# Kernel tuning notes

Hardware: AMD Instinct MI355X
Metric: run time of the kernel (lower is better)

Reference implementation:

```python
import jax, jax.numpy as jnp
import numpy as np

D_MODEL = 1024
NUM_HEADS = 16
D_K = D_MODEL // NUM_HEADS

def setup_inputs() -> dict:
    key = jax.random.key(0)
    ks = jax.random.split(key, 8)
    B, S, D = 2, 2048, D_MODEL
    scale = 1.0 / np.sqrt(D)
    return {
        "X_q": jax.random.normal(ks[0], (B, S, D), dtype=jnp.float32),
        "X_k": jax.random.normal(ks[1], (B, S, D), dtype=jnp.float32),
        "X_v": jax.random.normal(ks[2], (B, S, D), dtype=jnp.float32),
        "W_q": jax.random.normal(ks[3], (D, D), dtype=jnp.float32) * scale,
        "W_k": jax.random.normal(ks[4], (D, D), dtype=jnp.float32) * scale,
        "W_v": jax.random.normal(ks[5], (D, D), dtype=jnp.float32) * scale,
        "W_o": jax.random.normal(ks[6], (D, D), dtype=jnp.float32) * scale,
        "b_o": jnp.zeros((D,), dtype=jnp.float32),
    }

def reference(X_q, X_k, X_v, W_q, W_k, W_v, W_o, b_o):
    B, S, D = X_q.shape
    H, dk = NUM_HEADS, D_K
    # nn.Linear: x @ W.T
    Q = (X_q @ W_q.T).reshape(B, H, S, dk)  # faithful raw view, no transpose
    K = (X_k @ W_k.T).reshape(B, H, S, dk)
    V = (X_v @ W_v.T).reshape(B, H, S, dk)
    A = jnp.einsum("bhqd,bhkd->bhqk", Q, K) / np.sqrt(dk)  # [B,H,S,S]
    A = jax.nn.softmax(A, axis=-1)
    H_cat = jnp.einsum("bhqk,bhkd->bhqd", A, V).reshape(B, S, D)
    return H_cat @ W_o.T + b_o
```

## Files before the change

### kernel.cpp

```cpp
#include <hip/hip_runtime.h>

typedef __bf16 bf16;
typedef bf16 bf16x8 __attribute__((ext_vector_type(8)));
typedef bf16 bf16x4 __attribute__((ext_vector_type(4)));
typedef bf16 bf16x2 __attribute__((ext_vector_type(2)));
typedef float f32x4 __attribute__((ext_vector_type(4)));
typedef float f32x16 __attribute__((ext_vector_type(16)));
typedef int i32x4 __attribute__((ext_vector_type(4)));

#define XSZ 4194304
#define WSZ 1048576
#define KDIM 1024
#define QSCALE 0.1803368801111137f

__device__ __forceinline__ void async16(const bf16* g, bf16* l) {
  __builtin_amdgcn_global_load_lds(
      (const __attribute__((address_space(1))) unsigned int*)g,
      (__attribute__((address_space(3))) unsigned int*)l, 16, 0, 0);
}

__device__ __forceinline__ bf16x8 ld8(const bf16* p) {
  bf16x4 lo = *(const bf16x4*)p;
  bf16x4 hi = *(const bf16x4*)(p + 4);
  return __builtin_shufflevector(lo, hi, 0, 1, 2, 3, 4, 5, 6, 7);
}

__device__ __forceinline__ void st8s(bf16* p, bf16x8 v) {
  *(bf16x4*)p       = __builtin_shufflevector(v, v, 0, 1, 2, 3);
  *(bf16x4*)(p + 4) = __builtin_shufflevector(v, v, 4, 5, 6, 7);
}

__device__ __forceinline__ f32x4 mfma16(bf16x8 a, bf16x8 b, f32x4 c) {
  return __builtin_amdgcn_mfma_f32_16x16x32_bf16(a, b, c, 0, 0, 0);
}
__device__ __forceinline__ f32x16 mfma32(bf16x8 a, bf16x8 b, f32x16 c) {
  return __builtin_amdgcn_mfma_f32_32x32x16_bf16(a, b, c, 0, 0, 0);
}

__device__ __forceinline__ int packbf2(float lo, float hi) {
  bf16x2 t; t[0] = (bf16)lo; t[1] = (bf16)hi;
  return __builtin_bit_cast(int, t);
}

__device__ __forceinline__ float fast_exp2(float x) {
#if __has_builtin(__builtin_amdgcn_exp2f)
  return __builtin_amdgcn_exp2f(x);
#else
  return exp2f(x);
#endif
}


__global__ __launch_bounds__(256) void cast_all(const float* __restrict__ Xq, const float* __restrict__ Xk,
                                                const float* __restrict__ Xv, const float* __restrict__ Wq,
                                                const float* __restrict__ Wk, const float* __restrict__ Wv,
                                                const float* __restrict__ Wo, bf16* __restrict__ dst) {
  size_t i = ((size_t)blockIdx.x * 256 + threadIdx.x) * 8;
  const float* src; size_t off; float scale = 1.0f;
  if (i < XSZ)                { src = Xq; off = i; }
  else if (i < 2 * (size_t)XSZ) { src = Xk; off = i - XSZ; }
  else if (i < 3 * (size_t)XSZ) { src = Xv; off = i - 2 * (size_t)XSZ; }
  else if (i < 3 * (size_t)XSZ + WSZ) { src = Wq; off = i - 3 * (size_t)XSZ; scale = QSCALE; }
  else if (i < 3 * (size_t)XSZ + 2 * (size_t)WSZ) { src = Wk; off = i - 3 * (size_t)XSZ - WSZ; }
  else if (i < 3 * (size_t)XSZ + 3 * (size_t)WSZ) { src = Wv; off = i - 3 * (size_t)XSZ - 2 * (size_t)WSZ; }
  else                        { src = Wo; off = i - 3 * (size_t)XSZ - 3 * (size_t)WSZ; }
  float4 a = *(const float4*)(src + off);
  float4 b = *(const float4*)(src + off + 4);
  bf16x8 o;
  o[0] = (bf16)(a.x * scale); o[1] = (bf16)(a.y * scale);
  o[2] = (bf16)(a.z * scale); o[3] = (bf16)(a.w * scale);
  o[4] = (bf16)(b.x * scale); o[5] = (bf16)(b.y * scale);
  o[6] = (bf16)(b.z * scale); o[7] = (bf16)(b.w * scale);
  *(bf16x8*)(dst + i) = o;
}

__device__ __forceinline__ void gemm_nt_core(const bf16* __restrict__ A, const bf16* __restrict__ Bm,
                                             int m0, int n0, bf16* lds, f32x4 acc[4][4]) {
  const int t = threadIdx.x;
  const int lane = t & 63, wave = t >> 6;
  const int wm = wave & 1, wn = wave >> 1;
  const int quad = lane >> 4, m16 = lane & 15;
  bf16* As = lds;
  bf16* Bs = lds + 128 * 32;
  const int c0 = t, c1 = t + 256;
  const bf16* ga0 = A + (size_t)(m0 + (c0 >> 2)) * KDIM + (c0 & 3) * 8;
  const bf16* ga1 = A + (size_t)(m0 + (c1 >> 2)) * KDIM + (c1 & 3) * 8;
  const bf16* gb0 = Bm + (size_t)(n0 + (c0 >> 2)) * KDIM + (c0 & 3) * 8;
  const bf16* gb1 = Bm + (size_t)(n0 + (c1 >> 2)) * KDIM + (c1 & 3) * 8;
  for (int kt = 0; kt < KDIM; kt += 32) {
    async16(ga0 + kt, As + c0 * 8);
    async16(ga1 + kt, As + c1 * 8);
    async16(gb0 + kt, Bs + c0 * 8);
    async16(gb1 + kt, Bs + c1 * 8);
    __syncthreads();
    bf16x8 af[4], bfv[4];
    #pragma unroll
    for (int i = 0; i < 4; i++)
      af[i] = *(const bf16x8*)(As + (wm * 64 + i * 16 + m16) * 32 + quad * 8);
    #pragma unroll
    for (int i = 0; i < 4; i++)
      bfv[i] = *(const bf16x8*)(Bs + (wn * 64 + i * 16 + m16) * 32 + quad * 8);
    #pragma unroll
    for (int mi = 0; mi < 4; mi++)
      #pragma unroll
      for (int ni = 0; ni < 4; ni++)
        acc[mi][ni] = mfma16(af[mi], bfv[ni], acc[mi][ni]);
    __syncthreads();
  }
}

__global__ __launch_bounds__(256) void proj_gemm(const bf16* __restrict__ xq, const bf16* __restrict__ xk,
                                                 const bf16* __restrict__ xv, const bf16* __restrict__ wq,
                                                 const bf16* __restrict__ wk, const bf16* __restrict__ wv,
                                                 bf16* __restrict__ Qo, bf16* __restrict__ Ko,
                                                 bf16* __restrict__ Vo) {
  __shared__ bf16 lds[2 * 128 * 32];
  const int z = blockIdx.z;
  const bf16* A = (z == 0) ? xq : (z == 1) ? xk : xv;
  const bf16* W = (z == 0) ? wq : (z == 1) ? wk : wv;
  bf16* C = (z == 0) ? Qo : (z == 1) ? Ko : Vo;
  f32x4 acc[4][4];
  #pragma unroll
  for (int i = 0; i < 4; i++)
    #pragma unroll
    for (int j = 0; j < 4; j++) acc[i][j] = (f32x4){0.f, 0.f, 0.f, 0.f};
  gemm_nt_core(A, W, blockIdx.y * 128, blockIdx.x * 128, lds, acc);
  const int lane = threadIdx.x & 63, wave = threadIdx.x >> 6;
  const int wm = wave & 1, wn = wave >> 1, quad = lane >> 4, m16 = lane & 15;
  const int row0 = blockIdx.y * 128 + wm * 64;
  const int col0 = blockIdx.x * 128 + wn * 64;
  #pragma unroll
  for (int mi = 0; mi < 4; mi++)
    #pragma unroll
    for (int ni = 0; ni < 4; ni++)
      #pragma unroll
      for (int r = 0; r < 4; r++) {
        int row = row0 + mi * 16 + quad * 4 + r;
        int col = col0 + ni * 16 + m16;
        C[(size_t)row * 1024 + col] = (bf16)acc[mi][ni][r];
      }
}

__global__ __launch_bounds__(256) void out_gemm(const bf16* __restrict__ Hm, const bf16* __restrict__ wo,
                                                const float* __restrict__ bias, float* __restrict__ out) {
  __shared__ bf16 lds[128 * 32 + 64 * 32];
  bf16* As = lds;
  bf16* Bs = lds + 128 * 32;
  const int t = threadIdx.x;
  const int lane = t & 63, wave = t >> 6;
  const int wm = wave & 1, wn = wave >> 1;
  const int quad = lane >> 4, m16 = lane & 15;
  const int m0 = blockIdx.y * 128, n0 = blockIdx.x * 64;
  const int c0 = t, c1 = t + 256;
  const bf16* ga0 = Hm + (size_t)(m0 + (c0 >> 2)) * KDIM + (c0 & 3) * 8;
  const bf16* ga1 = Hm + (size_t)(m0 + (c1 >> 2)) * KDIM + (c1 & 3) * 8;
  const bf16* gb0 = wo + (size_t)(n0 + (c0 >> 2)) * KDIM + (c0 & 3) * 8;
  f32x4 acc[4][2];
  #pragma unroll
  for (int i = 0; i < 4; i++)
    #pragma unroll
    for (int j = 0; j < 2; j++) acc[i][j] = (f32x4){0.f, 0.f, 0.f, 0.f};
  for (int kt = 0; kt < KDIM; kt += 32) {
    async16(ga0 + kt, As + c0 * 8);
    async16(ga1 + kt, As + c1 * 8);
    if (c0 < 256) async16(gb0 + kt, Bs + c0 * 8);
    __syncthreads();
    bf16x8 af[4], bfv[2];
    #pragma unroll
    for (int i = 0; i < 4; i++)
      af[i] = *(const bf16x8*)(As + (wm * 64 + i * 16 + m16) * 32 + quad * 8);
    #pragma unroll
    for (int i = 0; i < 2; i++)
      bfv[i] = *(const bf16x8*)(Bs + (wn * 32 + i * 16 + m16) * 32 + quad * 8);
    #pragma unroll
    for (int mi = 0; mi < 4; mi++)
      #pragma unroll
      for (int ni = 0; ni < 2; ni++)
        acc[mi][ni] = mfma16(af[mi], bfv[ni], acc[mi][ni]);
    __syncthreads();
  }
  const int row0 = m0 + wm * 64;
  const int col0 = n0 + wn * 32;
  float bv[2];
  #pragma unroll
  for (int ni = 0; ni < 2; ni++) bv[ni] = bias[col0 + ni * 16 + m16];
  #pragma unroll
  for (int mi = 0; mi < 4; mi++)
    #pragma unroll
    for (int ni = 0; ni < 2; ni++)
      #pragma unroll
      for (int r = 0; r < 4; r++) {
        int row = row0 + mi * 16 + quad * 4 + r;
        int col = col0 + ni * 16 + m16;
        out[(size_t)row * 1024 + col] = acc[mi][ni][r] + bv[ni];
      }
}

__global__ __launch_bounds__(256) void transpose_v(const bf16* __restrict__ V, bf16* __restrict__ Vt) {
  __shared__ bf16 T[64 * 65];
  const int t = threadIdx.x;
  const bf16* src = V + (size_t)blockIdx.y * (2048 * 64) + (size_t)blockIdx.x * 64 * 64;
  bf16* dst = Vt + (size_t)blockIdx.y * (2048 * 64) + (size_t)blockIdx.x * 64;
  #pragma unroll
  for (int j = 0; j < 2; j++) {
    int c = t + j * 256;
    int row = c >> 3, col8 = (c & 7) * 8;
    bf16x8 v = *(const bf16x8*)(src + row * 64 + col8);
    #pragma unroll
    for (int i = 0; i < 8; i++) T[row * 65 + col8 + i] = v[i];
  }
  __syncthreads();
  #pragma unroll
  for (int j = 0; j < 2; j++) {
    int c = t + j * 256;
    int d = c >> 3, k8 = (c & 7) * 8;
    bf16x8 o;
    #pragma unroll
    for (int i = 0; i < 8; i++) o[i] = T[(k8 + i) * 65 + d];
    *(bf16x8*)(dst + (size_t)d * 2048 + k8) = o;
  }
}

#define KS 68
#define VS 132
#define HALF_LDS (128 * KS + 64 * VS)
__global__ __launch_bounds__(512, 2) void attn_kernel(const bf16* __restrict__ Qg,
                                                      const bf16* __restrict__ Kg,
                                                      const bf16* __restrict__ Vtg,
                                                      bf16* __restrict__ Hout) {
  __shared__ bf16 smem[2 * HALF_LDS];
  const int t = threadIdx.x;
  const int lane = t & 63;
  const int w = (t >> 6) & 3;
  const int half = t >> 8;
  const int tt = t & 255;
  const int l31 = lane & 31, h = lane >> 5;
  bf16* Ks = smem + half * HALF_LDS;
  bf16* Vs = Ks + 128 * KS;
  const int L = blockIdx.x + 16 * blockIdx.y;
  const int xcd = L & 7, j5 = L >> 3;
  const int bh = xcd * 4 + (j5 & 3);
  const int qt = j5 >> 2;
  const size_t base = (size_t)bh * (2048 * 64);
  const bf16* Kp = Kg + base;
  const bf16* Vp = Vtg + base;
  const int q = qt * 128 + w * 32 + l31;

  bf16x8 qf[4];
  #pragma unroll
  for (int kc = 0; kc < 4; kc++)
    qf[kc] = *(const bf16x8*)(Qg + base + (size_t)q * 64 + 16 * kc + 8 * h);

  f32x16 oacc[2];
  #pragma unroll
  for (int mt = 0; mt < 2; mt++)
    #pragma unroll
    for (int i = 0; i < 16; i++) oacc[mt][i] = 0.f;
  float lrow = 0.f;

  int krow[4], kcol[4], vrow[4], vcol[4];
  #pragma unroll
  for (int j = 0; j < 4; j++) {
    int c = tt + j * 256;
    krow[j] = c >> 3;  kcol[j] = (c & 7) * 8;
    vrow[j] = c >> 4;  vcol[j] = (c & 15) * 8;
  }

  const int tile0 = half * 8;
  bf16x8 kreg[4], vreg[4];
  #pragma unroll
  for (int j = 0; j < 4; j++) {
    kreg[j] = *(const bf16x8*)(Kp + (size_t)(tile0 * 128 + krow[j]) * 64 + kcol[j]);
    vreg[j] = *(const bf16x8*)(Vp + (size_t)vrow[j] * 2048 + tile0 * 128 + vcol[j]);
  }

  for (int kt = 0; kt < 8; kt++) {
    #pragma unroll
    for (int j = 0; j < 4; j++) st8s(Ks + krow[j] * KS + kcol[j], kreg[j]);
    #pragma unroll
    for (int j = 0; j < 4; j++) st8s(Vs + vrow[j] * VS + vcol[j], vreg[j]);
    __syncthreads();

    if (kt + 1 < 8) {
      const int tg = tile0 + kt + 1;
      #pragma unroll
      for (int j = 0; j < 4; j++) {
        kreg[j] = *(const bf16x8*)(Kp + (size_t)(tg * 128 + krow[j]) * 64 + kcol[j]);
        vreg[j] = *(const bf16x8*)(Vp + (size_t)vrow[j] * 2048 + tg * 128 + vcol[j]);
      }
    }

    #pragma unroll
    for (int mt = 0; mt < 4; mt++) {
      f32x16 sacc;
      #pragma unroll
      for (int i = 0; i < 16; i++) sacc[i] = 0.f;
      #pragma unroll
      for (int kc = 0; kc < 4; kc++) {
        bf16x8 kf = ld8(Ks + (32 * mt + l31) * KS + 16 * kc + 8 * h);
        sacc = mfma32(kf, qf[kc], sacc);
      }
      int pd[8];
      float sum = 0.f;
      #pragma unroll
      for (int p = 0; p < 8; p++) {
        float p0 = fast_exp2(sacc[2 * p]);
        float p1 = fast_exp2(sacc[2 * p + 1]);
        sum += p0 + p1;
        pd[p] = packbf2(p0, p1);
      }
      lrow += sum;
      #pragma unroll
      for (int c1 = 0; c1 < 2; c1++) {
        const int kc = 2 * mt + c1;
        const int rro = 2 * c1 + h;
        const int rrp = 2 * c1 + 1 - h;
        int s0 = __shfl_xor(pd[2 * rrp], 32, 64);
        int s1 = __shfl_xor(pd[2 * rrp + 1], 32, 64);
        int o0 = pd[2 * rro], o1 = pd[2 * rro + 1];
        i32x4 w4;
        w4.x = h ? s0 : o0;
        w4.y = h ? s1 : o1;
        w4.z = h ? o0 : s0;
        w4.w = h ? o1 : s1;
        bf16x8 pfrag = __builtin_bit_cast(bf16x8, w4);
        #pragma unroll
        for (int mtd = 0; mtd < 2; mtd++) {
          bf16x8 vf = ld8(Vs + (32 * mtd + l31) * VS + 16 * kc + 8 * h);
          oacc[mtd] = mfma32(vf, pfrag, oacc[mtd]);
        }
      }
    }
    __syncthreads();
  }

  lrow += __shfl_xor(lrow, 32, 64);
  float* Sf = (float*)smem;
  float* Tf = Sf + w * 2048;
  float* Lb = Sf + 8192 + w * 32;
  if (half) {
    #pragma unroll
    for (int mt = 0; mt < 2; mt++)
      #pragma unroll
      for (int r = 0; r < 16; r++) {
        int d = 32 * mt + (r & 3) + 8 * (r >> 2) + 4 * h;
        Tf[d * 32 + l31] = oacc[mt][r];
      }
    if (!h) Lb[l31] = lrow;
  }
  __syncthreads();
  if (!half) {
    float linv = 1.f / (lrow + Lb[l31]);
    #pragma unroll
    for (int mt = 0; mt < 2; mt++)
      #pragma unroll
      for (int r = 0; r < 16; r++) {
        int d = 32 * mt + (r & 3) + 8 * (r >> 2) + 4 * h;
        Tf[d * 32 + l31] = (oacc[mt][r] + Tf[d * 32 + l31]) * linv;
      }
  }
  __syncthreads();
  bf16* Hq = Hout + base + (size_t)(qt * 128 + w * 32 + l31) * 64 + 32 * h;
  #pragma unroll
  for (int s = 0; s < 2; s++) {
    int se = half * 2 + s;
    bf16x8 o;
    #pragma unroll
    for (int i = 0; i < 8; i++) o[i] = (bf16)Tf[(32 * h + se * 8 + i) * 32 + l31];
    *(bf16x8*)(Hq + se * 8) = o;
  }
}

extern "C" void kernel_launch(void* const* d_in, const int* in_sizes, int n_in,
                              void* d_out, int out_size, void* d_ws, size_t ws_size,
                              hipStream_t stream) {
  const float* Xq = (const float*)d_in[0];
  const float* Xk = (const float*)d_in[1];
  const float* Xv = (const float*)d_in[2];
  const float* Wq = (const float*)d_in[3];
  const float* Wk = (const float*)d_in[4];
  const float* Wv = (const float*)d_in[5];
  const float* Wo = (const float*)d_in[6];
  const float* bo = (const float*)d_in[7];

  bf16* ws = (bf16*)d_ws;
  bf16* xq = ws;
  bf16* xk = ws + XSZ;
  bf16* xv = ws + 2 * (size_t)XSZ;
  bf16* wq = ws + 3 * (size_t)XSZ;
  bf16* wk = wq + WSZ;
  bf16* wv = wk + WSZ;
  bf16* wo = wv + WSZ;
  bf16* q  = wo + WSZ;
  bf16* k  = q + XSZ;
  bf16* v  = k + XSZ;
  bf16* vt = xv;
  bf16* h  = xq;

  cast_all<<<8192, 256, 0, stream>>>(Xq, Xk, Xv, Wq, Wk, Wv, Wo, ws);
  proj_gemm<<<dim3(8, 32, 3), 256, 0, stream>>>(xq, xk, xv, wq, wk, wv, q, k, v);
  transpose_v<<<dim3(32, 32), 256, 0, stream>>>(v, vt);
  attn_kernel<<<dim3(16, 32), 512, 0, stream>>>(q, k, vt, h);
  out_gemm<<<dim3(16, 32), 256, 0, stream>>>(h, wo, bo, (float*)d_out);
}
```

Baseline: 245.4 us.

## Widen GEMM K-tile to 64 with XOR-swizzled LDS and raise MFMA priority

The projection and output GEMMs now stage 64-wide K tiles instead of 32, halving the number of barrier pairs per K loop. They also XOR-swizzle the LDS column layout so that 16-byte fragment reads avoid bank conflicts. Launch bounds request 3 blocks per CU, and the attention kernel wraps its MFMA sections in s_setprio so matrix work gets scheduling priority over other waves. The cost is doubled LDS per block, which may limit occupancy, and the swizzle must match exactly between global-to-LDS writes and fragment reads.

New measurement: 253.7 us. +3.4%, slower.

```diff
diff --git a/kernel.cpp b/kernel.cpp
--- a/kernel.cpp
+++ b/kernel.cpp
@@ -23,6 +23,10 @@
   bf16x4 lo = *(const bf16x4*)p;
   bf16x4 hi = *(const bf16x4*)(p + 4);
   return __builtin_shufflevector(lo, hi, 0, 1, 2, 3, 4, 5, 6, 7);
+}
+
+__device__ __forceinline__ bf16x8 ld16(const bf16* p) {
+  return __builtin_bit_cast(bf16x8, *(const i32x4*)p);
 }
 
 __device__ __forceinline__ void st8s(bf16* p, bf16x8 v) {
@@ -81,40 +85,49 @@
   const int wm = wave & 1, wn = wave >> 1;
   const int quad = lane >> 4, m16 = lane & 15;
   bf16* As = lds;
-  bf16* Bs = lds + 128 * 32;
-  const int c0 = t, c1 = t + 256;
-  const bf16* ga0 = A + (size_t)(m0 + (c0 >> 2)) * KDIM + (c0 & 3) * 8;
-  const bf16* ga1 = A + (size_t)(m0 + (c1 >> 2)) * KDIM + (c1 & 3) * 8;
-  const bf16* gb0 = Bm + (size_t)(n0 + (c0 >> 2)) * KDIM + (c0 & 3) * 8;
-  const bf16* gb1 = Bm + (size_t)(n0 + (c1 >> 2)) * KDIM + (c1 & 3) * 8;
-  for (int kt = 0; kt < KDIM; kt += 32) {
-    async16(ga0 + kt, As + c0 * 8);
-    async16(ga1 + kt, As + c1 * 8);
-    async16(gb0 + kt, Bs + c0 * 8);
-    async16(gb1 + kt, Bs + c1 * 8);
-    __syncthreads();
-    bf16x8 af[4], bfv[4];
-    #pragma unroll
-    for (int i = 0; i < 4; i++)
-      af[i] = *(const bf16x8*)(As + (wm * 64 + i * 16 + m16) * 32 + quad * 8);
-    #pragma unroll
-    for (int i = 0; i < 4; i++)
-      bfv[i] = *(const bf16x8*)(Bs + (wn * 64 + i * 16 + m16) * 32 + quad * 8);
-    #pragma unroll
-    for (int mi = 0; mi < 4; mi++)
-      #pragma unroll
-      for (int ni = 0; ni < 4; ni++)
-        acc[mi][ni] = mfma16(af[mi], bfv[ni], acc[mi][ni]);
-    __syncthreads();
-  }
-}
-
-__global__ __launch_bounds__(256) void proj_gemm(const bf16* __restrict__ xq, const bf16* __restrict__ xk,
+  bf16* Bs = lds + 128 * 64;
+  const bf16* gA[4]; int dstc[4];
+  #pragma unroll
+  for (int j = 0; j < 4; j++) {
+    int c = t + j * 256;
+    int row = c >> 3;
+    int col = ((c & 7) ^ (row & 7)) * 8;
+    gA[j] = A + (size_t)(m0 + row) * KDIM + col;
+    dstc[j] = c * 8;
+  }
+  const ptrdiff_t dBA = (Bm + (size_t)n0 * KDIM) - (A + (size_t)m0 * KDIM);
+  const int swz = (m16 & 7) * 8;
+  for (int kt = 0; kt < KDIM; kt += 64) {
+    #pragma unroll
+    for (int j = 0; j < 4; j++) async16(gA[j] + kt, As + dstc[j]);
+    #pragma unroll
+    for (int j = 0; j < 4; j++) async16(gA[j] + dBA + kt, Bs + dstc[j]);
+    __syncthreads();
+    #pragma unroll
+    for (int s = 0; s < 2; s++) {
+      bf16x8 af[4], bfv[4];
+      #pragma unroll
+      for (int i = 0; i < 4; i++)
+        af[i] = ld16(As + (wm * 64 + i * 16 + m16) * 64 + ((s * 32 + quad * 8) ^ swz));
+      #pragma unroll
+      for (int i = 0; i < 4; i++)
+        bfv[i] = ld16(Bs + (wn * 64 + i * 16 + m16) * 64 + ((s * 32 + quad * 8) ^ swz));
+      #pragma unroll
+      for (int mi = 0; mi < 4; mi++)
+        #pragma unroll
+        for (int ni = 0; ni < 4; ni++)
+          acc[mi][ni] = mfma16(af[mi], bfv[ni], acc[mi][ni]);
+    }
+    __syncthreads();
+  }
+}
+
+__global__ __launch_bounds__(256, 3) void proj_gemm(const bf16* __restrict__ xq, const bf16* __restrict__ xk,
                                                  const bf16* __restrict__ xv, const bf16* __restrict__ wq,
                                                  const bf16* __restrict__ wk, const bf16* __restrict__ wv,
                                                  bf16* __restrict__ Qo, bf16* __restrict__ Ko,
                                                  bf16* __restrict__ Vo) {
-  __shared__ bf16 lds[2 * 128 * 32];
+  __shared__ __align__(16) bf16 lds[2 * 128 * 64];
   const int z = blockIdx.z;
   const bf16* A = (z == 0) ? xq : (z == 1) ? xk : xv;
   const bf16* W = (z == 0) ? wq : (z == 1) ? wk : wv;
@@ -141,42 +154,61 @@
       }
 }
 
-__global__ __launch_bounds__(256) void out_gemm(const bf16* __restrict__ Hm, const bf16* __restrict__ wo,
+__global__ __launch_bounds__(256, 3) void out_gemm(const bf16* __restrict__ Hm, const bf16* __restrict__ wo,
                                                 const float* __restrict__ bias, float* __restrict__ out) {
-  __shared__ bf16 lds[128 * 32 + 64 * 32];
+  __shared__ __align__(16) bf16 lds[128 * 64 + 64 * 64];
   bf16* As = lds;
-  bf16* Bs = lds + 128 * 32;
+  bf16* Bs = lds + 128 * 64;
   const int t = threadIdx.x;
   const int lane = t & 63, wave = t >> 6;
   const int wm = wave & 1, wn = wave >> 1;
   const int quad = lane >> 4, m16 = lane & 15;
   const int m0 = blockIdx.y * 128, n0 = blockIdx.x * 64;
-  const int c0 = t, c1 = t + 256;
-  const bf16* ga0 = Hm + (size_t)(m0 + (c0 >> 2)) * KDIM + (c0 & 3) * 8;
-  const bf16* ga1 = Hm + (size_t)(m0 + (c1 >> 2)) * KDIM + (c1 & 3) * 8;
-  const bf16* gb0 = wo + (size_t)(n0 + (c0 >> 2)) * KDIM + (c0 & 3) * 8;
+  const bf16* gA[4]; int dstA[4];
+  #pragma unroll
+  for (int j = 0; j < 4; j++) {
+    int c = t + j * 256;
+    int row = c >> 3;
+    int col = ((c & 7) ^ (row & 7)) * 8;
+    gA[j] = Hm + (size_t)(m0 + row) * KDIM + col;
+    dstA[j] = c * 8;
+  }
+  const bf16* gB[2]; int dstB[2];
+  #pragma unroll
+  for (int j = 0; j < 2; j++) {
+    int c = t + j * 256;
+    int row = c >> 3;
+    int col = ((c & 7) ^ (row & 7)) * 8;
+    gB[j] = wo + (size_t)(n0 + row) * KDIM + col;
+    dstB[j] = c * 8;
+  }
+  const int swz = (m16 & 7) * 8;
   f32x4 acc[4][2];
   #pragma unroll
   for (int i = 0; i < 4; i++)
     #pragma unroll
     for (int j = 0; j < 2; j++) acc[i][j] = (f32x4){0.f, 0.f, 0.f, 0.f};
-  for (int kt = 0; kt < KDIM; kt += 32) {
-    async16(ga0 + kt, As + c0 * 8);
-    async16(ga1 + kt, As + c1 * 8);
-    if (c0 < 256) async16(gb0 + kt, Bs + c0 * 8);
-    __syncthreads();
-    bf16x8 af[4], bfv[2];
-    #pragma unroll
-    for (int i = 0; i < 4; i++)
-      af[i] = *(const bf16x8*)(As + (wm * 64 + i * 16 + m16) * 32 + quad * 8);
-    #pragma unroll
-    for (int i = 0; i < 2; i++)
-      bfv[i] = *(const bf16x8*)(Bs + (wn * 32 + i * 16 + m16) * 32 + quad * 8);
-    #pragma unroll
-    for (int mi = 0; mi < 4; mi++)
-      #pragma unroll
-      for (int ni = 0; ni < 2; ni++)
-        acc[mi][ni] = mfma16(af[mi], bfv[ni], acc[mi][ni]);
+  for (int kt = 0; kt < KDIM; kt += 64) {
+    #pragma unroll
+    for (int j = 0; j < 4; j++) async16(gA[j] + kt, As + dstA[j]);
+    #pragma unroll
+    for (int j = 0; j < 2; j++) async16(gB[j] + kt, Bs + dstB[j]);
+    __syncthreads();
+    #pragma unroll
+    for (int s = 0; s < 2; s++) {
+      bf16x8 af[4], bfv[2];
+      #pragma unroll
+      for (int i = 0; i < 4; i++)
+        af[i] = ld16(As + (wm * 64 + i * 16 + m16) * 64 + ((s * 32 + quad * 8) ^ swz));
+      #pragma unroll
+      for (int i = 0; i < 2; i++)
+        bfv[i] = ld16(Bs + (wn * 32 + i * 16 + m16) * 64 + ((s * 32 + quad * 8) ^ swz));
+      #pragma unroll
+      for (int mi = 0; mi < 4; mi++)
+        #pragma unroll
+        for (int ni = 0; ni < 2; ni++)
+          acc[mi][ni] = mfma16(af[mi], bfv[ni], acc[mi][ni]);
+    }
     __syncthreads();
   }
   const int row0 = m0 + wm * 64;
@@ -295,11 +327,13 @@
       f32x16 sacc;
       #pragma unroll
       for (int i = 0; i < 16; i++) sacc[i] = 0.f;
+      __builtin_amdgcn_s_setprio(1);
       #pragma unroll
       for (int kc = 0; kc < 4; kc++) {
         bf16x8 kf = ld8(Ks + (32 * mt + l31) * KS + 16 * kc + 8 * h);
         sacc = mfma32(kf, qf[kc], sacc);
       }
+      __builtin_amdgcn_s_setprio(0);
       int pd[8];
       float sum = 0.f;
       #pragma unroll
@@ -324,11 +358,13 @@
         w4.z = h ? o0 : s0;
         w4.w = h ? o1 : s1;
         bf16x8 pfrag = __builtin_bit_cast(bf16x8, w4);
+        __builtin_amdgcn_s_setprio(1);
         #pragma unroll
         for (int mtd = 0; mtd < 2; mtd++) {
           bf16x8 vf = ld8(Vs + (32 * mtd + l31) * VS + 16 * kc + 8 * h);
           oacc[mtd] = mfma32(vf, pfrag, oacc[mtd]);
         }
+        __builtin_amdgcn_s_setprio(0);
       }
     }
     __syncthreads();
```
